# Optimization experiments

Hardware: AMD Instinct MI355X
Metric: run time of the kernel (lower is better)

## Reference

```python
import jax, jax.numpy as jnp
import numpy as np

N_ROWS = 4096   # output features (N)
M_COLS = 4096   # input features (M)
BATCH = 4096
NNZ_PER_ROW = 819


def setup_inputs() -> dict:
    rng = np.random.default_rng(0)
    # sample NNZ_PER_ROW distinct, sorted column indices per row (CSR structure)
    cols = np.argsort(rng.random((N_ROWS, M_COLS)), axis=1)[:, :NNZ_PER_ROW]
    cols = np.sort(cols, axis=1).reshape(-1).astype(np.int32)            # [nnz]
    row_ids = np.repeat(np.arange(N_ROWS, dtype=np.int32), NNZ_PER_ROW)  # [nnz], expanded indptr

    key = jax.random.key(0)
    k1, k2, k3 = jax.random.split(key, 3)
    inp = jax.random.normal(k1, (BATCH, M_COLS), dtype=jnp.float32)
    W_val = jax.random.normal(k2, (N_ROWS * NNZ_PER_ROW,), dtype=jnp.float32) * 0.02
    bias = jax.random.normal(k3, (N_ROWS,), dtype=jnp.float32)
    return {
        "input": inp,
        "W_val": W_val,
        "bias": bias,
        "row_ids": jnp.asarray(row_ids),
        "cols": jnp.asarray(cols),
        "N": N_ROWS,
    }


def reference(input, W_val, bias, row_ids, cols, N):
    # Faithful math of SparseLinearFunction: y = x @ W^T + bias where W is the
    # CSR matrix (W_val, row_ids, cols) of shape (N, M). Densify via scatter
    # (CSR has unique (row, col) pairs) then use a single GEMM.
    M = input.shape[-1]
    W = jnp.zeros((N, M), dtype=W_val.dtype).at[row_ids, cols].set(W_val)  # [N, M]
    return jnp.matmul(input, W.T) + bias  # [B, N]
```

## Files before the change

kernel.cpp:

```cpp
#include <hip/hip_runtime.h>
#include <hip/hip_bf16.h>
#include <stdint.h>


#define B_DIM 4096
#define M_DIM 4096
#define N_DIM 4096
#define NNZ_ROW 819

typedef __attribute__((ext_vector_type(8))) __bf16 bf16x8;
typedef __attribute__((ext_vector_type(4))) float f32x4;

__device__ __forceinline__ unsigned short f32_to_bf16(float f) {
    union { float f; unsigned int u; } v;
    v.f = f;
    unsigned int r = v.u + 0x7FFFu + ((v.u >> 16) & 1u);
    return (unsigned short)(r >> 16);
}

__device__ __forceinline__ void load_lds16(const void* g, void* l) {
    __builtin_amdgcn_global_load_lds(
        (const __attribute__((address_space(1))) void*)g,
        (__attribute__((address_space(3))) void*)l,
        16, 0, 0);
}

__global__ __launch_bounds__(256) void prep(
    const float* __restrict__ wval,
    const int* __restrict__ cols,
    unsigned short* __restrict__ wb,
    const float4* __restrict__ x,
    uint4* __restrict__ xb) {
    const int tid = threadIdx.x;
    if (blockIdx.x >= N_DIM) {
        const int i = (blockIdx.x - N_DIM) * 256 + tid;
        const float4 a = x[2 * i];
        const float4 b = x[2 * i + 1];
        union { ushort ush[8]; uint4 u4; } o;
        o.ush[0] = f32_to_bf16(a.x); o.ush[1] = f32_to_bf16(a.y);
        o.ush[2] = f32_to_bf16(a.z); o.ush[3] = f32_to_bf16(a.w);
        o.ush[4] = f32_to_bf16(b.x); o.ush[5] = f32_to_bf16(b.y);
        o.ush[6] = f32_to_bf16(b.z); o.ush[7] = f32_to_bf16(b.w);
        xb[i] = o.u4;
        return;
    }
    __shared__ __attribute__((aligned(16))) unsigned short row_s[M_DIM];
    const int row = blockIdx.x;
    uint4* rs4 = (uint4*)row_s;
    rs4[tid]       = make_uint4(0u, 0u, 0u, 0u);
    rs4[tid + 256] = make_uint4(0u, 0u, 0u, 0u);
    __syncthreads();
    const size_t base = (size_t)row * NNZ_ROW;
    for (int j = tid; j < NNZ_ROW; j += 256) {
        const int c = cols[base + j];
        row_s[c] = f32_to_bf16(wval[base + j]);
    }
    __syncthreads();
    uint4* dst = (uint4*)(wb + (size_t)row * M_DIM);
    dst[tid]       = rs4[tid];
    dst[tid + 256] = rs4[tid + 256];
}

__device__ __forceinline__ void stage_half(
    const unsigned short* __restrict__ src,
    int grow0, int kt, unsigned short* dst, int w, int l) {
#pragma unroll
    for (int j = 0; j < 2; ++j) {
        const int seg = w * 2 + j;
        const int r   = seg * 8 + (l >> 3);
        const int cg  = (l >> 3) ^ (l & 7);
        load_lds16(src + (size_t)(grow0 + r) * M_DIM + kt + cg * 8,
                   dst + seg * 512);
    }
}

#define MFMA_STEP(ASET, BSET)                                                  \
    __builtin_amdgcn_s_setprio(1);                                             \
    _Pragma("unroll")                                                          \
    for (int mf = 0; mf < 4; ++mf)                                             \
        _Pragma("unroll")                                                      \
        for (int nf = 0; nf < 4; ++nf)                                         \
            acc[mf][nf] = __builtin_amdgcn_mfma_f32_16x16x32_bf16(             \
                ASET[mf], BSET[nf], acc[mf][nf], 0, 0, 0);                     \
    __builtin_amdgcn_s_setprio(0);

__device__ __forceinline__ void ktile(
    const unsigned short* As_c, const unsigned short* Bs_c,
    unsigned short* As_n, unsigned short* Bs_n,
    const unsigned short* __restrict__ Xb, const unsigned short* __restrict__ Wb,
    int bm0, int bn0, int knext, bool do_stage,
    int wr, int wc, int w, int l, f32x4 (&acc)[4][4])
{
    __builtin_amdgcn_s_waitcnt(0x0F70);
    __builtin_amdgcn_s_barrier();

    const int l15 = l & 15;
    const int lg  = l >> 4;
    const int lx  = l & 7;
    const int ck0 = (lg ^ lx) << 3;
    const int ck1 = ((4 + lg) ^ lx) << 3;

    const unsigned short* A0 = As_c + (wr * 64 + l15) * 64;
    const unsigned short* B0 = Bs_c + (wc * 64 + l15) * 64;

    if (do_stage) {
        stage_half(Xb, bm0,       knext, As_n,        w, l);
        stage_half(Wb, bn0,       knext, Bs_n,        w, l);
        stage_half(Wb, bn0 + 128, knext, Bs_n + 8192, w, l);
    }
    __builtin_amdgcn_sched_barrier(0);

    bf16x8 ak0[4], bk0[4], ak1[4], bk1[4];

#pragma unroll
    for (int mf = 0; mf < 4; ++mf)
        ak0[mf] = *(const bf16x8*)(A0 + mf * 1024 + ck0);
#pragma unroll
    for (int nf = 0; nf < 4; ++nf)
        bk0[nf] = *(const bf16x8*)(B0 + nf * 1024 + ck0);
    __builtin_amdgcn_sched_barrier(0);

#pragma unroll
    for (int mf = 0; mf < 4; ++mf)
        ak1[mf] = *(const bf16x8*)(A0 + mf * 1024 + ck1);
#pragma unroll
    for (int nf = 0; nf < 4; ++nf)
        bk1[nf] = *(const bf16x8*)(B0 + nf * 1024 + ck1);
    MFMA_STEP(ak0, bk0)
    __builtin_amdgcn_sched_barrier(0);

    MFMA_STEP(ak1, bk1)
    __builtin_amdgcn_sched_barrier(0);
}

__global__ __launch_bounds__(512, 2) void gemm_bt_bias(
    const unsigned short* __restrict__ Xb,
    const unsigned short* __restrict__ Wb,
    const float* __restrict__ bias,
    float* __restrict__ out)
{
    __shared__ __attribute__((aligned(16))) unsigned short As0[8192];
    __shared__ __attribute__((aligned(16))) unsigned short Bs0[16384];
    __shared__ __attribute__((aligned(16))) unsigned short As1[8192];
    __shared__ __attribute__((aligned(16))) unsigned short Bs1[16384];

    const int tid = threadIdx.x;
    const int w   = tid >> 6;
    const int l   = tid & 63;
    const int wr  = w >> 2;
    const int wc  = w & 3;

    const int wg  = blockIdx.y * 16 + blockIdx.x;
    const int idx = ((wg & 7) << 6) | (wg >> 3);
    const int bm0 = (idx >> 4) * 128;
    const int bn0 = (idx & 15) * 256;

    f32x4 acc[4][4];
#pragma unroll
    for (int a = 0; a < 4; ++a)
#pragma unroll
        for (int b = 0; b < 4; ++b) acc[a][b] = (f32x4)0.0f;

    stage_half(Xb, bm0,       0, As0,        w, l);
    stage_half(Wb, bn0,       0, Bs0,        w, l);
    stage_half(Wb, bn0 + 128, 0, Bs0 + 8192, w, l);

#pragma unroll 1
    for (int kt = 0; kt < M_DIM; kt += 128) {
        ktile(As0, Bs0, As1, Bs1, Xb, Wb, bm0, bn0, kt + 64, true,
              wr, wc, w, l, acc);
        ktile(As1, Bs1, As0, Bs0, Xb, Wb, bm0, bn0, kt + 128,
              kt + 128 < M_DIM, wr, wc, w, l, acc);
    }

    const int l15 = l & 15;
    const int lg  = l >> 4;
#pragma unroll
    for (int nf = 0; nf < 4; ++nf) {
        const int col = bn0 + wc * 64 + nf * 16 + l15;
        const float bv = bias[col];
#pragma unroll
        for (int mf = 0; mf < 4; ++mf) {
            const int row0 = bm0 + wr * 64 + mf * 16 + lg * 4;
#pragma unroll
            for (int r = 0; r < 4; ++r)
                out[(size_t)(row0 + r) * N_DIM + col] = acc[mf][nf][r] + bv;
        }
    }
}


extern "C" void kernel_launch(void* const* d_in, const int* in_sizes, int n_in,
                              void* d_out, int out_size, void* d_ws, size_t ws_size,
                              hipStream_t stream) {
    const float* x       = (const float*)d_in[0];
    const float* wval    = (const float*)d_in[1];
    const float* bias    = (const float*)d_in[2];
    const int*   cols    = (const int*)d_in[4];
    float* out = (float*)d_out;

    unsigned short* Wb = (unsigned short*)d_ws;
    unsigned short* Xb = Wb + (size_t)N_DIM * M_DIM;

    prep<<<dim3(N_DIM + (B_DIM * M_DIM) / 8 / 256), dim3(256), 0, stream>>>(
        wval, cols, Wb, (const float4*)x, (uint4*)Xb);
    gemm_bt_bias<<<dim3(N_DIM / 256, B_DIM / 128), dim3(512), 0, stream>>>(
        Xb, Wb, bias, out);
}
```

Measured before the change: 271.6 us.

## Restructure GEMM k-loop to prefetch LDS fragments across the barrier

The GEMM main loop is reorganised so the first k-half fragments of the next tile are read from LDS into registers while the current tile's second-half MFMAs run. There is now one wait-and-barrier per k-tile, and it sits after the first MFMA step instead of at the start. The prologue preloads two tiles, and global staging now overwrites the buffer just consumed. The aim is to hide LDS read latency behind MFMA work and to shorten the barrier stalls. The cost is extra register pressure from carrying fragments between tiles, and each wait still drains all outstanding global loads.

```diff
diff --git a/kernel.cpp b/kernel.cpp
--- a/kernel.cpp
+++ b/kernel.cpp
@@ -85,51 +85,52 @@
     __builtin_amdgcn_s_setprio(0);
 
 __device__ __forceinline__ void ktile(
-    const unsigned short* As_c, const unsigned short* Bs_c,
-    unsigned short* As_n, unsigned short* Bs_n,
+    unsigned short* curA, unsigned short* curB,
+    const unsigned short* nxtA, const unsigned short* nxtB,
     const unsigned short* __restrict__ Xb, const unsigned short* __restrict__ Wb,
-    int bm0, int bn0, int knext, bool do_stage,
-    int wr, int wc, int w, int l, f32x4 (&acc)[4][4])
+    int bm0, int bn0, int kstage, bool do_stage, bool do_next,
+    int wr, int wc, int w, int l,
+    bf16x8 (&ac)[4], bf16x8 (&bc)[4], f32x4 (&acc)[4][4])
 {
-    __builtin_amdgcn_s_waitcnt(0x0F70);
-    __builtin_amdgcn_s_barrier();
-
     const int l15 = l & 15;
     const int lg  = l >> 4;
     const int lx  = l & 7;
     const int ck0 = (lg ^ lx) << 3;
     const int ck1 = ((4 + lg) ^ lx) << 3;
 
-    const unsigned short* A0 = As_c + (wr * 64 + l15) * 64;
-    const unsigned short* B0 = Bs_c + (wc * 64 + l15) * 64;
+    const unsigned short* A0c = curA + (wr * 64 + l15) * 64;
+    const unsigned short* B0c = curB + (wc * 64 + l15) * 64;
+
+    bf16x8 an[4], bn[4];
+#pragma unroll
+    for (int mf = 0; mf < 4; ++mf)
+        an[mf] = *(const bf16x8*)(A0c + mf * 1024 + ck1);
+#pragma unroll
+    for (int nf = 0; nf < 4; ++nf)
+        bn[nf] = *(const bf16x8*)(B0c + nf * 1024 + ck1);
+    MFMA_STEP(ac, bc)
+    __builtin_amdgcn_sched_barrier(0);
+
+    __builtin_amdgcn_s_waitcnt(0x0070);
+    __builtin_amdgcn_s_barrier();
+    __builtin_amdgcn_sched_barrier(0);
 
     if (do_stage) {
-        stage_half(Xb, bm0,       knext, As_n,        w, l);
-        stage_half(Wb, bn0,       knext, Bs_n,        w, l);
-        stage_half(Wb, bn0 + 128, knext, Bs_n + 8192, w, l);
-    }
-    __builtin_amdgcn_sched_barrier(0);
-
-    bf16x8 ak0[4], bk0[4], ak1[4], bk1[4];
-
-#pragma unroll
-    for (int mf = 0; mf < 4; ++mf)
-        ak0[mf] = *(const bf16x8*)(A0 + mf * 1024 + ck0);
-#pragma unroll
-    for (int nf = 0; nf < 4; ++nf)
-        bk0[nf] = *(const bf16x8*)(B0 + nf * 1024 + ck0);
-    __builtin_amdgcn_sched_barrier(0);
-
-#pragma unroll
-    for (int mf = 0; mf < 4; ++mf)
-        ak1[mf] = *(const bf16x8*)(A0 + mf * 1024 + ck1);
-#pragma unroll
-    for (int nf = 0; nf < 4; ++nf)
-        bk1[nf] = *(const bf16x8*)(B0 + nf * 1024 + ck1);
-    MFMA_STEP(ak0, bk0)
-    __builtin_amdgcn_sched_barrier(0);
-
-    MFMA_STEP(ak1, bk1)
+        stage_half(Xb, bm0,       kstage, curA, w, l);
+        stage_half(Wb, bn0,       kstage, curB, w, l);
+        stage_half(Wb, bn0 + 128, kstage, curB + 8192, w, l);
+    }
+    if (do_next) {
+        const unsigned short* A0n = nxtA + (wr * 64 + l15) * 64;
+        const unsigned short* B0n = nxtB + (wc * 64 + l15) * 64;
+#pragma unroll
+        for (int mf = 0; mf < 4; ++mf)
+            ac[mf] = *(const bf16x8*)(A0n + mf * 1024 + ck0);
+#pragma unroll
+        for (int nf = 0; nf < 4; ++nf)
+            bc[nf] = *(const bf16x8*)(B0n + nf * 1024 + ck0);
+    }
+    MFMA_STEP(an, bn)
     __builtin_amdgcn_sched_barrier(0);
 }
 
@@ -161,20 +162,43 @@
 #pragma unroll
         for (int b = 0; b < 4; ++b) acc[a][b] = (f32x4)0.0f;
 
-    stage_half(Xb, bm0,       0, As0,        w, l);
-    stage_half(Wb, bn0,       0, Bs0,        w, l);
-    stage_half(Wb, bn0 + 128, 0, Bs0 + 8192, w, l);
-
-#pragma unroll 1
-    for (int kt = 0; kt < M_DIM; kt += 128) {
-        ktile(As0, Bs0, As1, Bs1, Xb, Wb, bm0, bn0, kt + 64, true,
-              wr, wc, w, l, acc);
-        ktile(As1, Bs1, As0, Bs0, Xb, Wb, bm0, bn0, kt + 128,
-              kt + 128 < M_DIM, wr, wc, w, l, acc);
-    }
-
     const int l15 = l & 15;
     const int lg  = l >> 4;
+    const int lx  = l & 7;
+    const int ck0 = (lg ^ lx) << 3;
+
+    stage_half(Xb, bm0,       0,  As0,        w, l);
+    stage_half(Wb, bn0,       0,  Bs0,        w, l);
+    stage_half(Wb, bn0 + 128, 0,  Bs0 + 8192, w, l);
+    stage_half(Xb, bm0,       64, As1,        w, l);
+    stage_half(Wb, bn0,       64, Bs1,        w, l);
+    stage_half(Wb, bn0 + 128, 64, Bs1 + 8192, w, l);
+    __builtin_amdgcn_s_waitcnt(0x0F70);
+    __builtin_amdgcn_s_barrier();
+
+    bf16x8 ac_[4], bc_[4];
+    {
+        const unsigned short* A0 = As0 + (wr * 64 + l15) * 64;
+        const unsigned short* B0 = Bs0 + (wc * 64 + l15) * 64;
+#pragma unroll
+        for (int mf = 0; mf < 4; ++mf)
+            ac_[mf] = *(const bf16x8*)(A0 + mf * 1024 + ck0);
+#pragma unroll
+        for (int nf = 0; nf < 4; ++nf)
+            bc_[nf] = *(const bf16x8*)(B0 + nf * 1024 + ck0);
+    }
+    __builtin_amdgcn_sched_barrier(0);
+
+#pragma unroll 1
+    for (int t = 0; t < 64; t += 2) {
+        ktile(As0, Bs0, As1, Bs1, Xb, Wb, bm0, bn0,
+              (t + 2) * 64, t + 2 < 64, true,
+              wr, wc, w, l, ac_, bc_, acc);
+        ktile(As1, Bs1, As0, Bs0, Xb, Wb, bm0, bn0,
+              (t + 3) * 64, t + 3 < 64, t + 1 < 63,
+              wr, wc, w, l, ac_, bc_, acc);
+    }
+
 #pragma unroll
     for (int nf = 0; nf < 4; ++nf) {
         const int col = bn0 + wc * 64 + nf * 16 + l15;
```

New measurement: 286.8 us. 1.06x slower.
